# Kernel optimization log

Measured on AMD Instinct MI355X. Metric: run time of the kernel, lower is better.

The kernel has to match this reference:

```python
import jax, jax.numpy as jnp
import numpy as np
import math


def _strided_value_mask(L, S, dtype):
    # mask_line[L + d] == 0 when |d| is a power-of-two stride in {2,4,...,<=L};
    # value_mask[i, j] = mask_line[L - i + j], i.e. zero where |j - i| is such a stride.
    diff = jnp.abs(jnp.arange(L)[:, None] - jnp.arange(S)[None, :])  # [L, S]
    vm = jnp.ones((L, S), dtype=dtype)
    stride = 2
    while stride <= L:
        vm = vm * (diff != stride).astype(dtype)
        stride *= 2
    return vm


def setup_inputs() -> dict:
    key = jax.random.key(0)
    k1, k2, k3 = jax.random.split(key, 3)
    B, L, H, E = 4, 2048, 8, 64
    D = 64
    return {
        "queries": jax.random.normal(k1, (B, L, H, E), dtype=jnp.float32),
        "keys": jax.random.normal(k2, (B, L, H, E), dtype=jnp.float32),
        "values": jax.random.normal(k3, (B, L, H, D), dtype=jnp.float32),
    }


def reference(queries, keys, values):
    B, L, H, E = queries.shape
    S = keys.shape[1]
    scale = 1.0 / math.sqrt(E)

    # raw scores [B, H, L, S]
    scores = jnp.einsum("blhe,bshe->bhls", queries, keys)
    # multiplicative strided mask (zeroes scores at power-of-two offsets)
    vm = _strided_value_mask(L, S, scores.dtype)  # [L, S]
    scores = scores * vm
    # causal mask: upper triangle -> -inf (mask_flag=True, attn_mask=None path)
    causal = jnp.triu(jnp.ones((L, S), dtype=bool), k=1)
    scores = jnp.where(causal, -jnp.inf, scores)

    # dropout p=0.0 (eval) -> identity
    A = jax.nn.softmax(scale * scores, axis=-1)
    V = jnp.einsum("bhls,bshd->blhd", A, values)
    return V
```

## Files before the change

### kernel.cpp

```cpp
#include <hip/hip_runtime.h>
#include <hip/hip_bf16.h>
#include <stdint.h>

typedef __attribute__((ext_vector_type(8))) short short8;
typedef __attribute__((ext_vector_type(16))) float f32x16;

namespace {
constexpr int NB = 4, NL = 2048, NH = 8, NE = 64, ND = 64;
constexpr float KS = 0.125f * 1.44269504f;
constexpr int RECSZ32 = 2080;
constexpr int NUNIT   = 160;
constexpr int NCHUNK = 40;
constexpr int RECSZ  = 8320;
constexpr int KSTEP  = 64 * NH * NE;
}

__device__ const unsigned char TG[40] = {
  3,7,7,10,11,11,11,14,14,15,15,15,15,
  6,6,9,9,10,10,12,12,13,13,13,13,14,14,
  2,5,5,8,8,8,9,12,12,
  4,4,1,0};
__device__ const unsigned char TT0[40] = {
  0,0,16,0,0,16,32,0,16,0,16,32,48,
  0,14,0,14,16,30,0,14,0,14,28,42,32,46,
  0,0,12,0,12,24,28,28,40,
  0,10,0,0};
__device__ const unsigned char TT1[40] = {
  16,16,32,16,16,32,48,16,32,16,32,48,64,
  14,28,14,28,30,44,14,28,14,28,42,56,46,60,
  12,12,24,12,24,36,40,40,52,
  10,20,8,4};
__device__ const unsigned char TREC[40] = {
  3,10,11,18,21,22,23,32,33,36,37,38,39,
  8,9,15,16,19,20,24,25,28,29,30,31,34,35,
  2,6,7,12,13,14,17,26,27,
  4,5,1,0};
__device__ const unsigned char CUMD[16] = {0,1,2,3,4,6,8,10,12,15,18,21,24,28,32,36};
__device__ const unsigned char NCHD[16] = {1,1,1,1,2,2,2,2,3,3,3,3,4,4,4,4};

__device__ __forceinline__ ushort bfb(float x) {
  __hip_bfloat16 b(x);
  return __builtin_bit_cast(ushort, b);
}
__device__ __forceinline__ uint32_t pkbf(float lo, float hi) {
  return (uint32_t)bfb(lo) | ((uint32_t)bfb(hi) << 16);
}


__global__ __launch_bounds__(256)
void convkv(const float* __restrict__ Kg, const float* __restrict__ Vg,
            char* __restrict__ kimg, char* __restrict__ vimg)
{
  const int id = blockIdx.x;
  const int kr = id & 31, bh = id >> 5;
  const int b = bh >> 3, h = bh & 7;
  const int tid = threadIdx.x;

  __shared__ float vt[64 * 64];

  const int key_in = tid >> 2;
  const int e0     = (tid & 3) * 16;
  {
    const float* vp = Vg + (((size_t)b * NL + kr * 64 + key_in) * NH + h) * ND + e0;
    float* dst = vt + key_in * 64 + e0;
    *(float4*)(dst)      = *(const float4*)(vp);
    *(float4*)(dst + 4)  = *(const float4*)(vp + 4);
    *(float4*)(dst + 8)  = *(const float4*)(vp + 8);
    *(float4*)(dst + 12) = *(const float4*)(vp + 12);
  }
  {
    const float* kp = Kg + (((size_t)b * NL + kr * 64 + key_in) * NH + h) * NE + e0;
    float4 a = *(const float4*)kp,      c = *(const float4*)(kp + 4);
    float4 d2 = *(const float4*)(kp + 8), f = *(const float4*)(kp + 12);
    uint4 wA = { pkbf(a.x,a.y), pkbf(a.z,a.w), pkbf(c.x,c.y), pkbf(c.z,c.w) };
    uint4 wB = { pkbf(d2.x,d2.y), pkbf(d2.z,d2.w), pkbf(f.x,f.y), pkbf(f.z,f.w) };
    char* ko = kimg + ((size_t)bh * 32 + kr) * 8192 + key_in * 128;
    const int C = (key_in & 7) << 4;
    *(uint4*)(ko + ((2 * e0)      ^ C)) = wA;
    *(uint4*)(ko + ((2 * e0 + 16) ^ C)) = wB;
  }
  __syncthreads();
  char* vo0 = vimg + ((size_t)bh * 32 + kr) * 8192;
  #pragma unroll
  for (int it = 0; it < 2; ++it) {
    int lin = it * 256 + tid;
    int d = lin & 63, kg = lin >> 6;
    const float* col = vt + kg * 8 * 64 + d;
    uint4 w = { pkbf(col[0], col[64]),    pkbf(col[128], col[192]),
                pkbf(col[256], col[320]), pkbf(col[384], col[448]) };
    *(uint4*)(vo0 + d * 128 + ((kg * 16) ^ ((d & 7) << 4))) = w;
  }
}

__global__ __launch_bounds__(256)
void sattn_wave(const float* __restrict__ Qg, const char* __restrict__ kimg,
                const char* __restrict__ vimg, float* __restrict__ W)
{
  const int id   = blockIdx.x;
  const int bh   = id & 31;
  const int ublk = id >> 5;
  const int b = bh >> 3, h = bh & 7;

  const int tid  = threadIdx.x;
  const int wave = tid >> 6;
  const int lane = tid & 63;
  const int ln31 = lane & 31;
  const int hi   = lane >> 5;

  const int u = ublk * 4 + wave;
  int G, s, k;
  if      (u < 16)  { G = 0; s = u;                 k = 0; }
  else if (u < 48)  { G = 1; s = 16 + (u - 16) / 2; k = (u - 16) % 2; }
  else if (u < 96)  { G = 2; s = 32 + (u - 48) / 3; k = (u - 48) % 3; }
  else              { G = 3; s = 48 + (u - 96) / 4; k = (u - 96) % 4; }
  (void)G;
  const int t0u = 16 * k;
  const int n   = s + 1;
  const int t1u = (16 * (k + 1) < n) ? 16 * (k + 1) : n;

  float* rec = W + ((size_t)bh * NUNIT + u) * RECSZ32;

  const int q0w = s * 32;
  const int qi  = q0w + ln31;
  const int rsw = (ln31 & 7) << 4;
  const char* kb_img = kimg + (size_t)bh * 32 * 8192;
  const char* vb_img = vimg + (size_t)bh * 32 * 8192;

  short8 qf[4];
  {
    const float* qp = Qg + (((size_t)b * NL + qi) * NH + h) * NE;
    #pragma unroll
    for (int st = 0; st < 4; ++st) {
      const float* qpe = qp + st * 16 + hi * 8;
      union { short8 v; uint32_t u[4]; } f;
      #pragma unroll
      for (int j = 0; j < 4; ++j)
        f.u[j] = pkbf(qpe[2 * j] * KS, qpe[2 * j + 1] * KS);
      qf[st] = f.v;
    }
  }

  f32x16 acc0, acc1;
  #pragma unroll
  for (int i = 0; i < 16; ++i) { acc0[i] = 0.f; acc1[i] = 0.f; }
  float ls = 0.f;

  for (int t = t0u; t < t1u; ++t) {
    const int kv0 = t * 32;
    const char* kbase = kb_img + (size_t)(t >> 1) * 8192 + ((t & 1) * 32 + ln31) * 128;
    const char* vbase = vb_img + (size_t)(t >> 1) * 8192;
    const int   vsub  = (t & 1) * 64;

    short8 a00 = *(const short8*)(vbase + ln31 * 128        + ((vsub      + hi * 16) ^ rsw));
    short8 a01 = *(const short8*)(vbase + ln31 * 128        + ((vsub + 32 + hi * 16) ^ rsw));
    short8 a10 = *(const short8*)(vbase + (32 + ln31) * 128 + ((vsub      + hi * 16) ^ rsw));
    short8 a11 = *(const short8*)(vbase + (32 + ln31) * 128 + ((vsub + 32 + hi * 16) ^ rsw));

    f32x16 sv;
    #pragma unroll
    for (int i = 0; i < 16; ++i) sv[i] = 0.f;
    #pragma unroll
    for (int st = 0; st < 4; ++st) {
      short8 kf = *(const short8*)(kbase + ((st * 32 + hi * 16) ^ rsw));
      sv = __builtin_amdgcn_mfma_f32_32x32x16_bf16(kf, qf[st], sv, 0, 0, 0);
    }

    const int delta = q0w - kv0;
    const int qrelh = (qi - kv0) - 4 * hi;
    float ps0 = 0.f, ps1 = 0.f;
    if (t == s) {
      #pragma unroll
      for (int r = 0; r < 16; ++r) {
        const int cr = (r & 3) + 8 * (r >> 2);
        int diff = qrelh - cr;
        float lg = sv[r];
        bool p2 = (diff > 1) & ((diff & (diff - 1)) == 0);
        lg = p2 ? 0.f : lg;
        lg = (diff < 0) ? -__builtin_inff() : lg;
        float p = exp2f(lg);
        sv[r] = p; (r & 1 ? ps1 : ps0) += p;
      }
    } else {
      int pmax = 1 << (31 - __clz(delta + 31));
      if (pmax >= delta - 31) {
        #pragma unroll
        for (int r = 0; r < 16; ++r) {
          const int cr = (r & 3) + 8 * (r >> 2);
          int diff = qrelh - cr;
          bool p2 = (diff > 1) & ((diff & (diff - 1)) == 0);
          float p = exp2f(p2 ? 0.f : sv[r]);
          sv[r] = p; (r & 1 ? ps1 : ps0) += p;
        }
      } else {
        #pragma unroll
        for (int r = 0; r < 16; ++r) {
          float p = exp2f(sv[r]);
          sv[r] = p; (r & 1 ? ps1 : ps0) += p;
        }
      }
    }
    ls += ps0 + ps1;

    uint32_t w0 = pkbf(sv[0],  sv[1]),  w1 = pkbf(sv[2],  sv[3]);
    uint32_t w2 = pkbf(sv[4],  sv[5]),  w3 = pkbf(sv[6],  sv[7]);
    uint32_t w4 = pkbf(sv[8],  sv[9]),  w5 = pkbf(sv[10], sv[11]);
    uint32_t w6 = pkbf(sv[12], sv[13]), w7 = pkbf(sv[14], sv[15]);
    uint32_t y0 = __shfl_xor(hi ? w0 : w2, 32);
    uint32_t y1 = __shfl_xor(hi ? w1 : w3, 32);
    uint32_t y2 = __shfl_xor(hi ? w4 : w6, 32);
    uint32_t y3 = __shfl_xor(hi ? w5 : w7, 32);
    union { short8 v; uint32_t u[4]; } f0, f1;
    if (hi == 0) {
      f0.u[0] = w0; f0.u[1] = w1; f0.u[2] = y0; f0.u[3] = y1;
      f1.u[0] = w4; f1.u[1] = w5; f1.u[2] = y2; f1.u[3] = y3;
    } else {
      f0.u[0] = y0; f0.u[1] = y1; f0.u[2] = w2; f0.u[3] = w3;
      f1.u[0] = y2; f1.u[1] = y3; f1.u[2] = w6; f1.u[3] = w7;
    }

    acc0 = __builtin_amdgcn_mfma_f32_32x32x16_bf16(a00, f0.v, acc0, 0, 0, 0);
    acc0 = __builtin_amdgcn_mfma_f32_32x32x16_bf16(a01, f1.v, acc0, 0, 0, 0);
    acc1 = __builtin_amdgcn_mfma_f32_32x32x16_bf16(a10, f0.v, acc1, 0, 0, 0);
    acc1 = __builtin_amdgcn_mfma_f32_32x32x16_bf16(a11, f1.v, acc1, 0, 0, 0);
  }

  ls += __shfl_xor(ls, 32);
  #pragma unroll
  for (int r = 0; r < 16; ++r) {
    int d = (r & 3) + 8 * (r >> 2) + 4 * hi;
    rec[d * 32 + ln31]        = acc0[r];
    rec[(32 + d) * 32 + ln31] = acc1[r];
  }
  if (hi == 0) rec[2048 + ln31] = ls;
}

__global__ __launch_bounds__(256)
void sattn_combine32(const float* __restrict__ W, float* __restrict__ Og)
{
  const int id = blockIdx.x;
  const int s  = id & 63, bh = id >> 6;
  const int b = bh >> 3, h = bh & 7;
  const int tid = threadIdx.x;

  const int G = s >> 4, i = s & 15;
  const int cum = 8 * G * (G + 1) + i * (G + 1);
  const int nc  = G + 1;
  const float* rec0 = W + ((size_t)bh * NUNIT + cum) * RECSZ32;

  __shared__ float sd[64][33];
  __shared__ float Lq[32];

  {
    int d = tid >> 2, q4 = (tid & 3) * 8;
    float4 a0 = {0,0,0,0}, a1 = {0,0,0,0};
    for (int c = 0; c < nc; ++c) {
      const float* rp = rec0 + (size_t)c * RECSZ32 + d * 32 + q4;
      float4 v0 = *(const float4*)rp, v1 = *(const float4*)(rp + 4);
      a0.x += v0.x; a0.y += v0.y; a0.z += v0.z; a0.w += v0.w;
      a1.x += v1.x; a1.y += v1.y; a1.z += v1.z; a1.w += v1.w;
    }
    sd[d][q4+0] = a0.x; sd[d][q4+1] = a0.y; sd[d][q4+2] = a0.z; sd[d][q4+3] = a0.w;
    sd[d][q4+4] = a1.x; sd[d][q4+5] = a1.y; sd[d][q4+6] = a1.z; sd[d][q4+7] = a1.w;
  }
  if (tid < 32) {
    float a = 0.f;
    for (int c = 0; c < nc; ++c) a += rec0[(size_t)c * RECSZ32 + 2048 + tid];
    Lq[tid] = 1.0f / a;
  }
  __syncthreads();
  {
    int q = tid >> 3, d8 = (tid & 7) * 8;
    float l = Lq[q];
    float4 o0 = { sd[d8+0][q]*l, sd[d8+1][q]*l, sd[d8+2][q]*l, sd[d8+3][q]*l };
    float4 o1 = { sd[d8+4][q]*l, sd[d8+5][q]*l, sd[d8+6][q]*l, sd[d8+7][q]*l };
    float* op = Og + (((size_t)b * NL + s * 32 + q) * NH + h) * ND + d8;
    *(float4*)op = o0; *(float4*)(op + 4) = o1;
  }
}

#define LD(RR) do {                                                         \
    const float* kp_ = kpp + (size_t)(RR) * KSTEP;                          \
    const float* vp_ = vpp + (size_t)(RR) * KSTEP;                          \
    kx0 = *(const float4*)(kp_);      kx1 = *(const float4*)(kp_ + 4);      \
    kx2 = *(const float4*)(kp_ + 8);  kx3 = *(const float4*)(kp_ + 12);     \
    vx0 = *(const float4*)(vp_);               vx1 = *(const float4*)(vp_ + NH*ND); \
    vx2 = *(const float4*)(vp_ + 2*NH*ND);     vx3 = *(const float4*)(vp_ + 3*NH*ND); \
  } while (0)

#define STG(KB, VB) do {                                                    \
    uint4 kwA = { pkbf(kx0.x,kx0.y), pkbf(kx0.z,kx0.w),                     \
                  pkbf(kx1.x,kx1.y), pkbf(kx1.z,kx1.w) };                   \
    uint4 kwB = { pkbf(kx2.x,kx2.y), pkbf(kx2.z,kx2.w),                     \
                  pkbf(kx3.x,kx3.y), pkbf(kx3.z,kx3.w) };                   \
    *(uint4*)((KB) + krow*128 + ( kcol2        ^ kswz)) = kwA;              \
    *(uint4*)((KB) + krow*128 + ((kcol2 + 16)  ^ kswz)) = kwB;              \
    _Pragma("unroll")                                                       \
    for (int j_ = 0; j_ < 4; ++j_) {                                        \
      int d_ = vd0 + j_;                                                    \
      char* vr_ = (VB) + d_*128;                                            \
      int vs_ = (d_ & 7) << 4;                                              \
      *(uint32_t*)(vr_ + ((vk0*2    ) ^ vs_)) = pkbf(vx0[j_], vx1[j_]);     \
      *(uint32_t*)(vr_ + ((vk0*2 + 4) ^ vs_)) = pkbf(vx2[j_], vx3[j_]);     \
    }                                                                       \
  } while (0)

#define COMPUTE(TT, SUB, KB, VB) do {                                       \
    const int kv0_ = (TT) * 32;                                             \
    f32x16 s;                                                               \
    _Pragma("unroll")                                                       \
    for (int i_ = 0; i_ < 16; ++i_) s[i_] = 0.f;                            \
    { const char* kb_ = (const char*)(KB) + ((SUB)*32 + ln31) * 128;        \
      _Pragma("unroll")                                                     \
      for (int st_ = 0; st_ < 4; ++st_) {                                   \
        short8 kf_ = *(const short8*)(kb_ + ((st_*32 + hi*16) ^ rsw));      \
        s = __builtin_amdgcn_mfma_f32_32x32x16_bf16(kf_, qf[st_], s, 0,0,0);\
      } }                                                                   \
    const int delta_ = q0w - kv0_;                                          \
    const int qrelh_ = (qi - kv0_) - 4 * hi;                                \
    if ((TT) == tw) {                                                       \
      _Pragma("unroll")                                                     \
      for (int r_ = 0; r_ < 16; ++r_) {                                     \
        const int cr_ = (r_ & 3) + 8 * (r_ >> 2);                           \
        int diff_ = qrelh_ - cr_;                                           \
        float lg_ = s[r_];                                                  \
        bool p2_ = (diff_ > 1) & ((diff_ & (diff_ - 1)) == 0);              \
        lg_ = p2_ ? 0.f : lg_;                                              \
        lg_ = (diff_ < 0) ? -__builtin_inff() : lg_;                        \
        s[r_] = exp2f(lg_);                                                 \
      }                                                                     \
    } else {                                                                \
      int pmax_ = 1 << (31 - __clz(delta_ + 31));                           \
      if (pmax_ >= delta_ - 31) {                                           \
        _Pragma("unroll")                                                   \
        for (int r_ = 0; r_ < 16; ++r_) {                                   \
          const int cr_ = (r_ & 3) + 8 * (r_ >> 2);                         \
          int diff_ = qrelh_ - cr_;                                         \
          bool p2_ = (diff_ > 1) & ((diff_ & (diff_ - 1)) == 0);            \
          s[r_] = exp2f(p2_ ? 0.f : s[r_]);                                 \
        }                                                                   \
      } else {                                                              \
        _Pragma("unroll")                                                   \
        for (int r_ = 0; r_ < 16; ++r_) s[r_] = exp2f(s[r_]);               \
      }                                                                     \
    }                                                                       \
    uint32_t w0_ = pkbf(s[0],  s[1]),  w1_ = pkbf(s[2],  s[3]);             \
    uint32_t w2_ = pkbf(s[4],  s[5]),  w3_ = pkbf(s[6],  s[7]);             \
    uint32_t w4_ = pkbf(s[8],  s[9]),  w5_ = pkbf(s[10], s[11]);            \
    uint32_t w6_ = pkbf(s[12], s[13]), w7_ = pkbf(s[14], s[15]);            \
    uint32_t y0_ = __shfl_xor(hi ? w0_ : w2_, 32);                          \
    uint32_t y1_ = __shfl_xor(hi ? w1_ : w3_, 32);                          \
    uint32_t y2_ = __shfl_xor(hi ? w4_ : w6_, 32);                          \
    uint32_t y3_ = __shfl_xor(hi ? w5_ : w7_, 32);                          \
    union { short8 v; uint32_t u[4]; } f0_, f1_;                            \
    if (hi == 0) {                                                          \
      f0_.u[0] = w0_; f0_.u[1] = w1_; f0_.u[2] = y0_; f0_.u[3] = y1_;       \
      f1_.u[0] = w4_; f1_.u[1] = w5_; f1_.u[2] = y2_; f1_.u[3] = y3_;       \
    } else {                                                                \
      f0_.u[0] = y0_; f0_.u[1] = y1_; f0_.u[2] = w2_; f0_.u[3] = w3_;       \
      f1_.u[0] = y2_; f1_.u[1] = y3_; f1_.u[2] = w6_; f1_.u[3] = w7_;       \
    }                                                                       \
    { const char* vr0_ = (const char*)(VB) + ln31 * 128;                    \
      const char* vr1_ = (const char*)(VB) + (32 + ln31) * 128;             \
      short8 a00_ = *(const short8*)(vr0_ + (((SUB)*64      + hi*16) ^ rsw));\
      short8 a01_ = *(const short8*)(vr0_ + (((SUB)*64 + 32 + hi*16) ^ rsw));\
      short8 a10_ = *(const short8*)(vr1_ + (((SUB)*64      + hi*16) ^ rsw));\
      short8 a11_ = *(const short8*)(vr1_ + (((SUB)*64 + 32 + hi*16) ^ rsw));\
      acc0 = __builtin_amdgcn_mfma_f32_32x32x16_bf16(a00_, f0_.v, acc0, 0,0,0); \
      acc0 = __builtin_amdgcn_mfma_f32_32x32x16_bf16(a01_, f1_.v, acc0, 0,0,0); \
      acc1 = __builtin_amdgcn_mfma_f32_32x32x16_bf16(a10_, f0_.v, acc1, 0,0,0); \
      acc1 = __builtin_amdgcn_mfma_f32_32x32x16_bf16(a11_, f1_.v, acc1, 0,0,0); \
      accl = __builtin_amdgcn_mfma_f32_32x32x16_bf16(onesv, f0_.v, accl, 0,0,0);\
      accl = __builtin_amdgcn_mfma_f32_32x32x16_bf16(onesv, f1_.v, accl, 0,0,0);\
    }                                                                       \
  } while (0)

__global__ __launch_bounds__(256, 3)
void sattn_mid(const float* __restrict__ Qg, const float* __restrict__ Kg,
               const float* __restrict__ Vg, float* __restrict__ W)
{
  const int id = blockIdx.x;
  const int bh = id & 31;
  const int e  = id >> 5;
  const int g  = TG[e];
  const int t0 = TT0[e], t1 = TT1[e];
  float* rec = W + (size_t)(bh * NCHUNK + TREC[e]) * RECSZ;
  const int b = bh >> 3, h = bh & 7;

  const int tid  = threadIdx.x;
  const int wave = tid >> 6;
  const int lane = tid & 63;
  const int ln31 = lane & 31;
  const int hi   = lane >> 5;

  __shared__ __align__(16) struct { ushort kt[64 * 64]; ushort vt[64 * 64]; } lds;

  const int q0w = g * 128 + wave * 32;
  const int qi  = q0w + ln31;
  const int tw  = 4 * g + wave;
  const int rsw = (ln31 & 7) << 4;

  short8 qf[4];
  {
    const float* qp = Qg + (((size_t)b * NL + qi) * NH + h) * NE;
    #pragma unroll
    for (int st = 0; st < 4; ++st) {
      const float* qpe = qp + st * 16 + hi * 8;
      union { short8 v; uint32_t u[4]; } f;
      #pragma unroll
      for (int j = 0; j < 4; ++j)
        f.u[j] = pkbf(qpe[2 * j] * KS, qpe[2 * j + 1] * KS);
      qf[st] = f.v;
    }
  }
  short8 onesv;
  {
    union { short8 v; uint32_t u[4]; } o;
    #pragma unroll
    for (int j = 0; j < 4; ++j) o.u[j] = 0x3F803F80u;
    onesv = o.v;
  }

  f32x16 acc0, acc1, accl;
  #pragma unroll
  for (int i = 0; i < 16; ++i) { acc0[i] = 0.f; acc1[i] = 0.f; accl[i] = 0.f; }

  const int krow = tid >> 2,        kcol = (tid & 3) * 16;
  const int vk0  = (tid & 15) * 4,  vd0  = (tid >> 4) * 4;
  const int kbase = t0 * 32;
  const float* kpp = Kg + (((size_t)b * NL + kbase + krow) * NH + h) * NE + kcol;
  const float* vpp = Vg + (((size_t)b * NL + kbase + vk0 ) * NH + h) * ND + vd0;
  const int kswz  = (krow & 7) << 4;
  const int kcol2 = kcol * 2;

  float4 kx0, kx1, kx2, kx3, vx0, vx1, vx2, vx3;

  const int nr = (t1 - t0) >> 1;
  LD(0);
  STG((char*)lds.kt, (char*)lds.vt);
  __syncthreads();
  if (nr > 1) LD(1);
  for (int r = 0;;) {
    const int tt = t0 + 2 * r;
    if (tt     <= tw) COMPUTE(tt,     0, (char*)lds.kt, (char*)lds.vt);
    if (tt + 1 <= tw) COMPUTE(tt + 1, 1, (char*)lds.kt, (char*)lds.vt);
    if (++r == nr) break;
    __syncthreads();
    STG((char*)lds.kt, (char*)lds.vt);
    __syncthreads();
    if (r + 1 < nr) LD(r + 1);
  }

  #pragma unroll
  for (int r = 0; r < 16; ++r) {
    int d = (r & 3) + 8 * (r >> 2) + 4 * hi;
    rec[d * 128 + wave * 32 + ln31]        = acc0[r];
    rec[(32 + d) * 128 + wave * 32 + ln31] = acc1[r];
  }
  if (hi == 0) rec[8192 + wave * 32 + ln31] = accl[0];
}

__global__ __launch_bounds__(256)
void sattn_combine(const float* __restrict__ W, float* __restrict__ Og)
{
  const int id = blockIdx.x;
  const int h2 = id & 1, g = (id >> 1) & 15, bh = id >> 5;
  const int b = bh >> 3, h = bh & 7;
  const int tid = threadIdx.x;

  __shared__ float sd[64][67];
  __shared__ float Lq[64];

  const float* rec0 = W + (size_t)(bh * NCHUNK + CUMD[g]) * RECSZ;
  const int nc = NCHD[g];

  #pragma unroll
  for (int rep = 0; rep < 4; ++rep) {
    int d  = rep * 16 + (tid >> 4);
    int q4 = (tid & 15) * 4;
    float4 a = {0.f, 0.f, 0.f, 0.f};
    for (int c = 0; c < nc; ++c) {
      float4 v = *(const float4*)(rec0 + (size_t)c * RECSZ + d * 128 + h2 * 64 + q4);
      a.x += v.x; a.y += v.y; a.z += v.z; a.w += v.w;
    }
    sd[d][q4 + 0] = a.x; sd[d][q4 + 1] = a.y;
    sd[d][q4 + 2] = a.z; sd[d][q4 + 3] = a.w;
  }
  if (tid < 64) {
    float a = 0.f;
    for (int c = 0; c < nc; ++c) a += rec0[(size_t)c * RECSZ + 8192 + h2 * 64 + tid];
    Lq[tid] = 1.0f / a;
  }
  __syncthreads();
  #pragma unroll
  for (int rep = 0; rep < 4; ++rep) {
    int q  = rep * 16 + (tid >> 4);
    int d4 = (tid & 15) * 4;
    float l = Lq[q];
    float4 o = { sd[d4][q] * l, sd[d4 + 1][q] * l, sd[d4 + 2][q] * l, sd[d4 + 3][q] * l };
    *(float4*)(Og + (((size_t)b * NL + g * 128 + h2 * 64 + q) * NH + h) * ND + d4) = o;
  }
}

extern "C" void kernel_launch(void* const* d_in, const int* in_sizes, int n_in,
                              void* d_out, int out_size, void* d_ws, size_t ws_size,
                              hipStream_t stream) {
  const float* Q = (const float*)d_in[0];
  const float* K = (const float*)d_in[1];
  const float* V = (const float*)d_in[2];
  float* O = (float*)d_out;
  const size_t recbytes = (size_t)32 * NUNIT * RECSZ32 * sizeof(float);
  const size_t imgsz    = (size_t)32 * 32 * 8192;
  const size_t need_full = recbytes + 2 * imgsz;
  const size_t need_mid  = (size_t)32 * NCHUNK * RECSZ * sizeof(float);
  float* W = (float*)d_ws;
  if (ws_size >= need_full) {
    char* kimg = (char*)d_ws + recbytes;
    char* vimg = kimg + imgsz;
    convkv        <<<dim3(1024), dim3(256), 0, stream>>>(K, V, kimg, vimg);
    sattn_wave    <<<dim3(1280), dim3(256), 0, stream>>>(Q, kimg, vimg, W);
    sattn_combine32<<<dim3(2048), dim3(256), 0, stream>>>(W, O);
  } else {
    sattn_mid     <<<dim3(32 * NCHUNK), dim3(256), 0, stream>>>(Q, K, V, W);
    sattn_combine <<<dim3(1024), dim3(256), 0, stream>>>(W, O);
  }
}
```

Baseline: 73.18 us.

## Pre-arrange K/V into per-lane MFMA fragment order and reorder wave work units

The conversion kernel now writes K and V as bf16 images laid out in exact MFMA fragment order, so each lane reads contiguous 16-byte chunks at fixed offsets. This drops the XOR-swizzled address math in the attention loop and makes the global loads fully coalesced. A lookup table also remaps blocks to work units so each block mixes long and short query rows, which balances per-block load, while the record index keeps the layout the combine kernel expects. The cost is an extra shared-memory staging pass for K in the conversion kernel.

```diff
diff --git a/kernel.cpp b/kernel.cpp
--- a/kernel.cpp
+++ b/kernel.cpp
@@ -14,6 +14,19 @@
 constexpr int RECSZ  = 8320;
 constexpr int KSTEP  = 64 * NH * NE;
 }
+
+__device__ const unsigned char TBL[160] = {
+  15,16,17,18,  19,20,21,22,  23,24,25,26,  27,28,29,30,
+  31,95,32,96,  33,97,34,98,  35,99,36,100, 37,101,38,102,
+  39,103,40,104, 41,105,42,106, 43,107,44,108, 45,109,46,110,
+  47,111,175,48, 112,176,49,113, 177,50,114,178, 51,115,179,52,
+  116,180,53,117, 181,54,118,182, 55,119,183,56, 120,184,57,121,
+  185,58,122,186, 59,123,187,60, 124,188,61,125, 189,62,126,190,
+  63,127,191,255,
+  0,94,160,254,  1,93,161,253,  2,92,162,252,  3,91,163,251,
+  4,90,164,250,  5,89,165,249,  6,88,166,248,  7,87,167,247,
+  8,86,168,246,  9,85,169,245, 10,84,170,244, 11,83,171,243,
+  12,82,172,242, 13,81,173,241, 14,80,174,240};
 
 __device__ const unsigned char TG[40] = {
   3,7,7,10,11,11,11,14,14,15,15,15,15,
@@ -48,52 +61,67 @@
 
 
 __global__ __launch_bounds__(256)
-void convkv(const float* __restrict__ Kg, const float* __restrict__ Vg,
-            char* __restrict__ kimg, char* __restrict__ vimg)
+void convfrag(const float* __restrict__ Kg, const float* __restrict__ Vg,
+              char* __restrict__ kimg, char* __restrict__ vimg)
 {
   const int id = blockIdx.x;
   const int kr = id & 31, bh = id >> 5;
   const int b = bh >> 3, h = bh & 7;
   const int tid = threadIdx.x;
 
-  __shared__ float vt[64 * 64];
-
-  const int key_in = tid >> 2;
-  const int e0     = (tid & 3) * 16;
-  {
-    const float* vp = Vg + (((size_t)b * NL + kr * 64 + key_in) * NH + h) * ND + e0;
-    float* dst = vt + key_in * 64 + e0;
+  __shared__ __align__(16) char  kt[64 * 128];
+  __shared__ __align__(16) float vt[64 * 64];
+
+  const int key = tid >> 2;
+  const int e0  = (tid & 3) * 16;
+  {
+    const float* kp = Kg + (((size_t)b * NL + kr * 64 + key) * NH + h) * NE + e0;
+    float4 a = *(const float4*)kp,       c = *(const float4*)(kp + 4);
+    float4 d2 = *(const float4*)(kp + 8), f = *(const float4*)(kp + 12);
+    uint4 wA = { pkbf(a.x,a.y), pkbf(a.z,a.w), pkbf(c.x,c.y), pkbf(c.z,c.w) };
+    uint4 wB = { pkbf(d2.x,d2.y), pkbf(d2.z,d2.w), pkbf(f.x,f.y), pkbf(f.z,f.w) };
+    const int sw = (key & 7) << 4;
+    *(uint4*)(kt + key * 128 + ((2 * e0)      ^ sw)) = wA;
+    *(uint4*)(kt + key * 128 + ((2 * e0 + 16) ^ sw)) = wB;
+  }
+  {
+    const float* vp = Vg + (((size_t)b * NL + kr * 64 + key) * NH + h) * ND + e0;
+    float* dst = vt + key * 64 + e0;
     *(float4*)(dst)      = *(const float4*)(vp);
     *(float4*)(dst + 4)  = *(const float4*)(vp + 4);
     *(float4*)(dst + 8)  = *(const float4*)(vp + 8);
     *(float4*)(dst + 12) = *(const float4*)(vp + 12);
   }
-  {
-    const float* kp = Kg + (((size_t)b * NL + kr * 64 + key_in) * NH + h) * NE + e0;
-    float4 a = *(const float4*)kp,      c = *(const float4*)(kp + 4);
-    float4 d2 = *(const float4*)(kp + 8), f = *(const float4*)(kp + 12);
-    uint4 wA = { pkbf(a.x,a.y), pkbf(a.z,a.w), pkbf(c.x,c.y), pkbf(c.z,c.w) };
-    uint4 wB = { pkbf(d2.x,d2.y), pkbf(d2.z,d2.w), pkbf(f.x,f.y), pkbf(f.z,f.w) };
-    char* ko = kimg + ((size_t)bh * 32 + kr) * 8192 + key_in * 128;
-    const int C = (key_in & 7) << 4;
-    *(uint4*)(ko + ((2 * e0)      ^ C)) = wA;
-    *(uint4*)(ko + ((2 * e0 + 16) ^ C)) = wB;
-  }
   __syncthreads();
-  char* vo0 = vimg + ((size_t)bh * 32 + kr) * 8192;
+
+  char* kob = kimg + (size_t)bh * 262144 + (size_t)kr * 2 * 4096;
+  char* vob = vimg + (size_t)bh * 262144 + (size_t)kr * 2 * 4096;
   #pragma unroll
   for (int it = 0; it < 2; ++it) {
     int lin = it * 256 + tid;
-    int d = lin & 63, kg = lin >> 6;
-    const float* col = vt + kg * 8 * 64 + d;
-    uint4 w = { pkbf(col[0], col[64]),    pkbf(col[128], col[192]),
-                pkbf(col[256], col[320]), pkbf(col[384], col[448]) };
-    *(uint4*)(vo0 + d * 128 + ((kg * 16) ^ ((d & 7) << 4))) = w;
+    int fi = lin >> 6, l = lin & 63;
+    int tt = fi >> 2, st = fi & 3;
+    int ky = tt * 32 + (l & 31);
+    int e  = st * 16 + (l >> 5) * 8;
+    uint4 w = *(const uint4*)(kt + ky * 128 + ((2 * e) ^ ((ky & 7) << 4)));
+    *(uint4*)(kob + tt * 4096 + st * 1024 + l * 16) = w;
+  }
+  #pragma unroll
+  for (int it = 0; it < 2; ++it) {
+    int lin = it * 256 + tid;
+    int fi = lin >> 6, l = lin & 63;
+    int tt = fi >> 2, f = fi & 3;
+    int d  = (f >> 1) * 32 + (l & 31);
+    int k0 = tt * 32 + (f & 1) * 16 + (l >> 5) * 8;
+    const float* c0 = vt + k0 * 64 + d;
+    uint4 w = { pkbf(c0[0],   c0[64]),  pkbf(c0[128], c0[192]),
+                pkbf(c0[256], c0[320]), pkbf(c0[384], c0[448]) };
+    *(uint4*)(vob + tt * 4096 + f * 1024 + l * 16) = w;
   }
 }
 
 __global__ __launch_bounds__(256)
-void sattn_wave(const float* __restrict__ Qg, const char* __restrict__ kimg,
+void sattn_frag(const float* __restrict__ Qg, const char* __restrict__ kimg,
                 const char* __restrict__ vimg, float* __restrict__ W)
 {
   const int id   = blockIdx.x;
@@ -107,24 +135,18 @@
   const int ln31 = lane & 31;
   const int hi   = lane >> 5;
 
-  const int u = ublk * 4 + wave;
-  int G, s, k;
-  if      (u < 16)  { G = 0; s = u;                 k = 0; }
-  else if (u < 48)  { G = 1; s = 16 + (u - 16) / 2; k = (u - 16) % 2; }
-  else if (u < 96)  { G = 2; s = 32 + (u - 48) / 3; k = (u - 48) % 3; }
-  else              { G = 3; s = 48 + (u - 96) / 4; k = (u - 96) % 4; }
-  (void)G;
-  const int t0u = 16 * k;
-  const int n   = s + 1;
-  const int t1u = (16 * (k + 1) < n) ? 16 * (k + 1) : n;
-
-  float* rec = W + ((size_t)bh * NUNIT + u) * RECSZ32;
+  const int e   = TBL[ublk * 4 + wave];
+  const int s   = e & 63, k = e >> 6;
+  const int t0u = k * 16;
+  const int t1u = (t0u + 16 < s + 1) ? t0u + 16 : s + 1;
+  const int G   = s >> 4;
+  const int rix = 8 * G * (G + 1) + (s & 15) * (G + 1) + k;
+  float* rec = W + ((size_t)bh * NUNIT + rix) * RECSZ32;
 
   const int q0w = s * 32;
   const int qi  = q0w + ln31;
-  const int rsw = (ln31 & 7) << 4;
-  const char* kb_img = kimg + (size_t)bh * 32 * 8192;
-  const char* vb_img = vimg + (size_t)bh * 32 * 8192;
+  const char* kb_img = kimg + (size_t)bh * 262144 + lane * 16;
+  const char* vb_img = vimg + (size_t)bh * 262144 + lane * 16;
 
   short8 qf[4];
   {
@@ -146,25 +168,26 @@
   float ls = 0.f;
 
   for (int t = t0u; t < t1u; ++t) {
-    const int kv0 = t * 32;
-    const char* kbase = kb_img + (size_t)(t >> 1) * 8192 + ((t & 1) * 32 + ln31) * 128;
-    const char* vbase = vb_img + (size_t)(t >> 1) * 8192;
-    const int   vsub  = (t & 1) * 64;
-
-    short8 a00 = *(const short8*)(vbase + ln31 * 128        + ((vsub      + hi * 16) ^ rsw));
-    short8 a01 = *(const short8*)(vbase + ln31 * 128        + ((vsub + 32 + hi * 16) ^ rsw));
-    short8 a10 = *(const short8*)(vbase + (32 + ln31) * 128 + ((vsub      + hi * 16) ^ rsw));
-    short8 a11 = *(const short8*)(vbase + (32 + ln31) * 128 + ((vsub + 32 + hi * 16) ^ rsw));
+    const char* kp = kb_img + (size_t)t * 4096;
+    const char* vp = vb_img + (size_t)t * 4096;
+    short8 a00 = *(const short8*)(vp);
+    short8 a01 = *(const short8*)(vp + 1024);
+    short8 a10 = *(const short8*)(vp + 2048);
+    short8 a11 = *(const short8*)(vp + 3072);
+    short8 kf0 = *(const short8*)(kp);
+    short8 kf1 = *(const short8*)(kp + 1024);
+    short8 kf2 = *(const short8*)(kp + 2048);
+    short8 kf3 = *(const short8*)(kp + 3072);
 
     f32x16 sv;
     #pragma unroll
     for (int i = 0; i < 16; ++i) sv[i] = 0.f;
-    #pragma unroll
-    for (int st = 0; st < 4; ++st) {
-      short8 kf = *(const short8*)(kbase + ((st * 32 + hi * 16) ^ rsw));
-      sv = __builtin_amdgcn_mfma_f32_32x32x16_bf16(kf, qf[st], sv, 0, 0, 0);
-    }
-
+    sv = __builtin_amdgcn_mfma_f32_32x32x16_bf16(kf0, qf[0], sv, 0, 0, 0);
+    sv = __builtin_amdgcn_mfma_f32_32x32x16_bf16(kf1, qf[1], sv, 0, 0, 0);
+    sv = __builtin_amdgcn_mfma_f32_32x32x16_bf16(kf2, qf[2], sv, 0, 0, 0);
+    sv = __builtin_amdgcn_mfma_f32_32x32x16_bf16(kf3, qf[3], sv, 0, 0, 0);
+
+    const int kv0 = t * 32;
     const int delta = q0w - kv0;
     const int qrelh = (qi - kv0) - 4 * hi;
     float ps0 = 0.f, ps1 = 0.f;
@@ -509,18 +532,17 @@
   const float* V = (const float*)d_in[2];
   float* O = (float*)d_out;
   const size_t recbytes = (size_t)32 * NUNIT * RECSZ32 * sizeof(float);
-  const size_t imgsz    = (size_t)32 * 32 * 8192;
+  const size_t imgsz    = (size_t)32 * 64 * 4096;
   const size_t need_full = recbytes + 2 * imgsz;
-  const size_t need_mid  = (size_t)32 * NCHUNK * RECSZ * sizeof(float);
   float* W = (float*)d_ws;
   if (ws_size >= need_full) {
     char* kimg = (char*)d_ws + recbytes;
     char* vimg = kimg + imgsz;
-    convkv        <<<dim3(1024), dim3(256), 0, stream>>>(K, V, kimg, vimg);
-    sattn_wave    <<<dim3(1280), dim3(256), 0, stream>>>(Q, kimg, vimg, W);
+    convfrag       <<<dim3(1024), dim3(256), 0, stream>>>(K, V, kimg, vimg);
+    sattn_frag     <<<dim3(1280), dim3(256), 0, stream>>>(Q, kimg, vimg, W);
     sattn_combine32<<<dim3(2048), dim3(256), 0, stream>>>(W, O);
   } else {
-    sattn_mid     <<<dim3(32 * NCHUNK), dim3(256), 0, stream>>>(Q, K, V, W);
-    sattn_combine <<<dim3(1024), dim3(256), 0, stream>>>(W, O);
-  }
-}
+    sattn_mid      <<<dim3(32 * NCHUNK), dim3(256), 0, stream>>>(Q, K, V, W);
+    sattn_combine  <<<dim3(1024), dim3(256), 0, stream>>>(W, O);
+  }
+}
```

After: 70.60 us. -3.5%, faster.
